# Optimization experiments

Measured on AMD Instinct MI355X. Metric: run time of the kernel, lower is better.

The kernel has to match this reference:

```python
import math
import jax, jax.numpy as jnp
import numpy as np

B, T, C, H = 2, 4096, 512, 8  # batch, seq_len, n_embd, n_head
D = C // H                    # head_dim = 64

def setup_inputs() -> dict:
    key = jax.random.key(0)
    k1, k2, k3 = jax.random.split(key, 3)
    x = jax.random.normal(k1, (B, T, C), dtype=jnp.float32)
    # torch Linear(C, 3C, bias=False): y = x @ W.T; we store the transposed
    # weight directly so the forward is x @ W_attn.
    W_attn = jax.random.normal(k2, (C, 3 * C), dtype=jnp.float32) * 0.02
    W_proj = jax.random.normal(k3, (C, C), dtype=jnp.float32) * 0.02
    return {"x": x, "W_attn": W_attn, "W_proj": W_proj}

def reference(x, W_attn, W_proj):
    b, t, c = x.shape
    # fused QKV projection, split like .split(n_embd, dim=2)
    qkv = x @ W_attn                              # [B,T,3C]
    q, k, v = jnp.split(qkv, 3, axis=-1)          # each [B,T,C]
    def to_heads(u):
        return u.reshape(b, t, H, D).transpose(0, 2, 1, 3)  # [B,H,T,D]
    q, k, v = to_heads(q), to_heads(k), to_heads(v)
    scale = 1.0 / math.sqrt(D)
    att = jnp.einsum('bhqd,bhkd->bhqk', q, k) * scale       # [B,H,T,T]
    causal = jnp.tril(jnp.ones((t, t), dtype=bool))         # masked_fill(triu(...,1), -inf)
    att = jnp.where(causal, att, -jnp.inf)
    probs = jax.nn.softmax(att, axis=-1)
    y = jnp.einsum('bhqk,bhkd->bhqd', probs, v)             # [B,H,T,D]
    y = y.transpose(0, 2, 1, 3).reshape(b, t, c)            # [B,T,C]
    return y @ W_proj
```

## Files before the change

### kernel.cpp

```cpp
#include <hip/hip_runtime.h>
#include <hip/hip_bf16.h>
#include <stdint.h>


typedef __attribute__((ext_vector_type(8))) short short8;
typedef __attribute__((ext_vector_type(4))) float floatx4;
typedef __attribute__((ext_vector_type(16))) float floatx16;
#if __has_builtin(__builtin_amdgcn_permlane32_swap)
typedef __attribute__((ext_vector_type(2))) unsigned int uint2v;
#define HAVE_PLSWAP 1
#else
#define HAVE_PLSWAP 0
#endif

__device__ __forceinline__ unsigned short f2bf(float f) {
    unsigned int x = __float_as_uint(f);
    unsigned int r = x + 0x7fffu + ((x >> 16) & 1u);
    return (unsigned short)(r >> 16);
}

__device__ __forceinline__ unsigned int pk_bf16(float a, float b) {
    __hip_bfloat162 p = __float22bfloat162_rn(make_float2(a, b));
    return *reinterpret_cast<unsigned int*>(&p);
}

__device__ __forceinline__ void gl_lds16(const unsigned short* g, unsigned char* l) {
    __builtin_amdgcn_global_load_lds(
        (const __attribute__((address_space(1))) unsigned int*)g,
        (__attribute__((address_space(3))) unsigned int*)l, 16, 0, 0);
}

__global__ __launch_bounds__(256) void prep_a(
    const float* __restrict__ x, unsigned short* __restrict__ xb,
    const float* __restrict__ Wa, unsigned short* __restrict__ WaT)
{
    const int bid = blockIdx.x;
    const int tid = threadIdx.x;
    if (bid < 2048) {
        size_t i = ((size_t)bid * 256 + tid) * 8;
        float4 a = *reinterpret_cast<const float4*>(x + i);
        float4 b = *reinterpret_cast<const float4*>(x + i + 4);
        unsigned short o[8] = {f2bf(a.x), f2bf(a.y), f2bf(a.z), f2bf(a.w),
                               f2bf(b.x), f2bf(b.y), f2bf(b.z), f2bf(b.w)};
        *reinterpret_cast<uint4*>(xb + i) = *reinterpret_cast<uint4*>(o);
    } else {
        __shared__ unsigned short tile[32][34];
        const int t2 = bid - 2048;
        const int n0 = (t2 % 48) * 32, k0 = (t2 / 48) * 32;
        const int tx = tid & 31, ty = tid >> 5;
        #pragma unroll
        for (int p = 0; p < 4; ++p)
            tile[tx][ty + p * 8] = f2bf(Wa[(size_t)(k0 + ty + p * 8) * 1536 + n0 + tx]);
        __syncthreads();
        #pragma unroll
        for (int p = 0; p < 4; ++p)
            WaT[(size_t)(n0 + ty + p * 8) * 512 + k0 + tx] = tile[ty + p * 8][tx];
    }
}

__global__ __launch_bounds__(256) void transpose_wp(
    const float* __restrict__ W, unsigned short* __restrict__ Wt)
{
    __shared__ unsigned short tile[32][34];
    const int tid = threadIdx.x;
    const int tx = tid & 31, ty = tid >> 5;
    const int n0 = blockIdx.x * 32, k0 = blockIdx.y * 32;
    #pragma unroll
    for (int p = 0; p < 4; ++p)
        tile[tx][ty + p * 8] = f2bf(W[(size_t)(k0 + ty + p * 8) * 512 + n0 + tx]);
    __syncthreads();
    #pragma unroll
    for (int p = 0; p < 4; ++p)
        Wt[(size_t)(n0 + ty + p * 8) * 512 + k0 + tx] = tile[ty + p * 8][tx];
}

template<int EPI>
__global__ __launch_bounds__(256) void mm_bt(
    const unsigned short* __restrict__ A,
    const unsigned short* __restrict__ Bt,
    void* __restrict__ outp)
{
    __shared__ __align__(16) unsigned char smem[40960];

    const int tid  = threadIdx.x;
    const int wave = tid >> 6;
    const int lane = tid & 63;
    const int quad = lane >> 4;
    const int l16  = lane & 15;
    const int wr   = wave >> 1;
    const int wc   = wave & 1;
    const int m0 = blockIdx.x * 128;
    const int n0 = blockIdx.y * 128;

    floatx4 acc[4][4];
    #pragma unroll
    for (int i = 0; i < 4; ++i)
        #pragma unroll
        for (int j = 0; j < 4; ++j) acc[i][j] = (floatx4){0.f, 0.f, 0.f, 0.f};

    const unsigned short* aS = A  + (size_t)(m0 + wave * 16 + (lane >> 2)) * 512 + (lane & 3) * 8;
    const unsigned short* bS = Bt + (size_t)(n0 + wave * 16 + (lane >> 2)) * 512 + (lane & 3) * 8;

#define STAGE(K0S, BUF)                                                     \
    {   unsigned char* Ab = smem + (BUF) * 16384 + wave * 1024;             \
        gl_lds16(aS + (K0S),             Ab);                               \
        gl_lds16(aS + (K0S) + 64 * 512,  Ab + 4096);                        \
        gl_lds16(bS + (K0S),             Ab + 8192);                        \
        gl_lds16(bS + (K0S) + 64 * 512,  Ab + 12288);                       \
    }

    STAGE(0, 0);

    for (int it = 0; it < 16; ++it) {
        __syncthreads();
        if (it < 15) STAGE((it + 1) * 32, (it & 1) ^ 1);

        const unsigned char* Al = smem + (it & 1) * 16384;
        const unsigned char* Bl = Al + 8192;

        short8 af[4], bf[4];
        #pragma unroll
        for (int ti = 0; ti < 4; ++ti)
            af[ti] = *reinterpret_cast<const short8*>(
                Al + (wr * 64 + ti * 16 + l16) * 64 + quad * 16);
        #pragma unroll
        for (int tj = 0; tj < 4; ++tj)
            bf[tj] = *reinterpret_cast<const short8*>(
                Bl + (wc * 64 + tj * 16 + l16) * 64 + quad * 16);
        #pragma unroll
        for (int ti = 0; ti < 4; ++ti)
            #pragma unroll
            for (int tj = 0; tj < 4; ++tj)
                acc[ti][tj] = __builtin_amdgcn_mfma_f32_16x16x32_bf16(af[ti], bf[tj], acc[ti][tj], 0, 0, 0);
    }
#undef STAGE

    if (EPI == 0) {
        unsigned short* WS = (unsigned short*)outp;
        unsigned short* Qb  = WS;
        unsigned short* Kb  = WS + 4194304;
        unsigned short* Vtb = WS + 8388608;
        const int which = n0 >> 9;
        const int h = ((n0 + wc * 64) >> 6) & 7;

        if (which == 2) {
            auto Tr = reinterpret_cast<unsigned short(*)[80]>(smem);
            __syncthreads();
            #pragma unroll
            for (int ti = 0; ti < 4; ++ti)
                #pragma unroll
                for (int tj = 0; tj < 4; ++tj) {
                    unsigned int lo = pk_bf16(acc[ti][tj][0], acc[ti][tj][1]);
                    unsigned int hi = pk_bf16(acc[ti][tj][2], acc[ti][tj][3]);
                    *reinterpret_cast<uint2*>(&Tr[(wave << 6) + tj * 16 + l16][ti * 16 + quad * 4])
                        = make_uint2(lo, hi);
                }
            const int b = m0 >> 12;
            const int bh = b * 8 + h;
            const int t0g = (m0 & 4095) + wr * 64;
            const int tseg = (lane & 7) * 8;
            #pragma unroll
            for (int p = 0; p < 8; ++p) {
                int dl = p * 8 + (lane >> 3);
                uint4 v = *reinterpret_cast<const uint4*>(&Tr[(wave << 6) + dl][tseg]);
                *reinterpret_cast<uint4*>(&Vtb[((size_t)(bh * 64 + dl)) * 4096 + t0g + tseg]) = v;
            }
        } else {
            const float sc = (which == 0) ? 0.18033688f : 1.0f;
            #pragma unroll
            for (int ti = 0; ti < 4; ++ti) {
                #pragma unroll
                for (int r = 0; r < 4; ++r) {
                    int m = m0 + wr * 64 + ti * 16 + quad * 4 + r;
                    int b = m >> 12, t = m & 4095;
                    int bh = b * 8 + h;
                    #pragma unroll
                    for (int tj = 0; tj < 4; ++tj) {
                        int d = tj * 16 + l16;
                        unsigned short val = f2bf(acc[ti][tj][r] * sc);
                        if (which == 0) Qb[((size_t)bh * 4096 + t) * 64 + d] = val;
                        else            Kb[((size_t)bh * 4096 + t) * 64 + d] = val;
                    }
                }
            }
        }
    } else {
        float* Out = (float*)outp;
        #pragma unroll
        for (int ti = 0; ti < 4; ++ti) {
            #pragma unroll
            for (int r = 0; r < 4; ++r) {
                int m = m0 + wr * 64 + ti * 16 + quad * 4 + r;
                #pragma unroll
                for (int tj = 0; tj < 4; ++tj) {
                    int n = n0 + wc * 64 + tj * 16 + l16;
                    Out[(size_t)m * 512 + n] = acc[ti][tj][r];
                }
            }
        }
    }
}

__global__ __launch_bounds__(256) void attn_mfma(
    const unsigned short* __restrict__ Q,
    const unsigned short* __restrict__ K,
    const unsigned short* __restrict__ Vt,
    unsigned short* __restrict__ Y)
{
    __shared__ __align__(16) unsigned short Kc[2][64][64];
    __shared__ __align__(16) unsigned short Vc[2][64][64];

    const int tid  = threadIdx.x;
    const int wave = tid >> 6;
    const int lane = tid & 63;
    const int l32  = lane & 31;
    const int hh   = lane >> 5;
    const int swz  = l32 & 7;
    const int p    = wave >> 1;
    const int w    = wave & 1;

    const int bid = blockIdx.x;
    const int bh  = bid & 15;
    const int j   = (bid >> 4) & 15;
    const int g   = bid >> 8;
    const int qb  = (g == 0) ? j : (g == 1) ? (63 - j) : (g == 2) ? (16 + j) : (47 - j);
    const int m0  = qb * 64;

    const unsigned short* Qp = Q  + (size_t)bh * (4096 * 64);
    const unsigned short* Kp = K  + (size_t)bh * (4096 * 64);
    const unsigned short* Vp = Vt + (size_t)bh * (64 * 4096);

    short8 qf[4];
    #pragma unroll
    for (int k16 = 0; k16 < 4; ++k16)
        qf[k16] = *reinterpret_cast<const short8*>(
            &Qp[(size_t)(m0 + 32 * p + l32) * 64 + k16 * 16 + hh * 8]);

    short8 ones;
    #pragma unroll
    for (int i = 0; i < 8; ++i) ones[i] = (short)0x3F80;

    floatx16 o0 = {0,0,0,0,0,0,0,0,0,0,0,0,0,0,0,0};
    floatx16 o1 = {0,0,0,0,0,0,0,0,0,0,0,0,0,0,0,0};
    floatx16 o4 = {0,0,0,0,0,0,0,0,0,0,0,0,0,0,0,0};

    const int rr  = tid >> 3;
    const int cc  = tid & 7;
    const int c0  = cc * 8;
    const int scs = ((cc ^ (rr & 7)) << 3);

    uint4 rk0 = *reinterpret_cast<const uint4*>(&Kp[(size_t)rr * 64 + c0]);
    uint4 rk1 = *reinterpret_cast<const uint4*>(&Kp[(size_t)(rr + 32) * 64 + c0]);
    uint4 rv0 = *reinterpret_cast<const uint4*>(&Vp[(size_t)rr * 4096 + c0]);
    uint4 rv1 = *reinterpret_cast<const uint4*>(&Vp[(size_t)(rr + 32) * 4096 + c0]);
    *reinterpret_cast<uint4*>(&Kc[0][rr][scs])      = rk0;
    *reinterpret_cast<uint4*>(&Kc[0][rr + 32][scs]) = rk1;
    *reinterpret_cast<uint4*>(&Vc[0][rr][scs])      = rv0;
    *reinterpret_cast<uint4*>(&Vc[0][rr + 32][scs]) = rv1;

    const unsigned short* kq0 = Kp + (size_t)(64 + rr) * 64 + c0;
    const unsigned short* kq1 = Kp + (size_t)(64 + rr + 32) * 64 + c0;
    const unsigned short* vq0 = Vp + (size_t)rr * 4096 + 64 + c0;
    const unsigned short* vq1 = Vp + (size_t)(rr + 32) * 4096 + 64 + c0;

    const int NT = qb + 1;
    for (int kt = 0; kt < NT; ++kt) {
        __syncthreads();
        const int cur = kt & 1;
        const int nxt = cur ^ 1;

        if (kt + 1 < NT) {
            rk0 = *reinterpret_cast<const uint4*>(kq0);
            rk1 = *reinterpret_cast<const uint4*>(kq1);
            rv0 = *reinterpret_cast<const uint4*>(vq0);
            rv1 = *reinterpret_cast<const uint4*>(vq1);
            kq0 += 4096; kq1 += 4096; vq0 += 64; vq1 += 64;
        }

        const bool active = (kt < qb) || (w == 0) || (p == 1);
        if (active) {
            floatx16 s = {0,0,0,0,0,0,0,0,0,0,0,0,0,0,0,0};
            #pragma unroll
            for (int k16 = 0; k16 < 4; ++k16) {
                const int chs = ((2 * k16 + hh) ^ swz) << 3;
                short8 a = *reinterpret_cast<const short8*>(&Kc[cur][32 * w + l32][chs]);
                s = __builtin_amdgcn_mfma_f32_32x32x16_bf16(a, qf[k16], s, 0, 0, 0);
            }
            if (kt == qb) {
                const int ql = 32 * p + l32;
                #pragma unroll
                for (int r = 0; r < 16; ++r) {
                    const int kl = 32 * w + (r & 3) + 8 * (r >> 2) + 4 * hh;
                    s[r] = (kl <= ql) ? s[r] : -1e30f;
                }
            }
            #pragma unroll
            for (int r = 0; r < 16; ++r) s[r] = __builtin_amdgcn_exp2f(s[r]);

            unsigned int A0 = pk_bf16(s[0],  s[1]),  B0 = pk_bf16(s[2],  s[3]);
            unsigned int A1 = pk_bf16(s[4],  s[5]),  B1 = pk_bf16(s[6],  s[7]);
            unsigned int A2 = pk_bf16(s[8],  s[9]),  B2 = pk_bf16(s[10], s[11]);
            unsigned int A3 = pk_bf16(s[12], s[13]), B3 = pk_bf16(s[14], s[15]);
            short8 pa[2];
#if HAVE_PLSWAP
            {
                uint2v rA = __builtin_amdgcn_permlane32_swap(A0, A1, false, false);
                uint2v rB = __builtin_amdgcn_permlane32_swap(B0, B1, false, false);
                uint4 u0 = make_uint4(rA[0], rB[0], rA[1], rB[1]);
                pa[0] = *reinterpret_cast<short8*>(&u0);
                rA = __builtin_amdgcn_permlane32_swap(A2, A3, false, false);
                rB = __builtin_amdgcn_permlane32_swap(B2, B3, false, false);
                uint4 u1 = make_uint4(rA[0], rB[0], rA[1], rB[1]);
                pa[1] = *reinterpret_cast<short8*>(&u1);
            }
#else
            {
                unsigned int pA0 = __shfl_xor((int)A0, 32), pA1 = __shfl_xor((int)A1, 32);
                unsigned int pB0 = __shfl_xor((int)B0, 32), pB1 = __shfl_xor((int)B1, 32);
                unsigned int pA2 = __shfl_xor((int)A2, 32), pA3 = __shfl_xor((int)A3, 32);
                unsigned int pB2 = __shfl_xor((int)B2, 32), pB3 = __shfl_xor((int)B3, 32);
                uint4 u0 = make_uint4(hh ? pA1 : A0, hh ? pB1 : B0,
                                      hh ? A1 : pA0, hh ? B1 : pB0);
                pa[0] = *reinterpret_cast<short8*>(&u0);
                uint4 u1 = make_uint4(hh ? pA3 : A2, hh ? pB3 : B2,
                                      hh ? A3 : pA2, hh ? B3 : pB2);
                pa[1] = *reinterpret_cast<short8*>(&u1);
            }
#endif
            o4 = __builtin_amdgcn_mfma_f32_32x32x16_bf16(pa[0], ones, o4, 0, 0, 0);
            o4 = __builtin_amdgcn_mfma_f32_32x32x16_bf16(pa[1], ones, o4, 0, 0, 0);

            #pragma unroll
            for (int f = 0; f < 2; ++f) {
                const int chs = ((4 * w + 2 * f + hh) ^ swz) << 3;
                short8 b0 = *reinterpret_cast<const short8*>(&Vc[cur][l32][chs]);
                short8 b1 = *reinterpret_cast<const short8*>(&Vc[cur][32 + l32][chs]);
                o0 = __builtin_amdgcn_mfma_f32_32x32x16_bf16(pa[f], b0, o0, 0, 0, 0);
                o1 = __builtin_amdgcn_mfma_f32_32x32x16_bf16(pa[f], b1, o1, 0, 0, 0);
            }
        }

        if (kt + 1 < NT) {
            *reinterpret_cast<uint4*>(&Kc[nxt][rr][scs])      = rk0;
            *reinterpret_cast<uint4*>(&Kc[nxt][rr + 32][scs]) = rk1;
            *reinterpret_cast<uint4*>(&Vc[nxt][rr][scs])      = rv0;
            *reinterpret_cast<uint4*>(&Vc[nxt][rr + 32][scs]) = rv1;
        }
    }

    __syncthreads();
    float* Ob  = reinterpret_cast<float*>(&Kc[0][0][0]);
    float* Wsf = reinterpret_cast<float*>(&Vc[0][0][0]);
    if (l32 == 0) {
        #pragma unroll
        for (int r = 0; r < 16; ++r) {
            const int qloc = (r & 3) + 8 * (r >> 2) + 4 * hh;
            Wsf[(p * 2 + w) * 32 + qloc] = o4[r];
        }
    }
    #pragma unroll
    for (int r = 0; r < 16; ++r) {
        const int qloc = (r & 3) + 8 * (r >> 2) + 4 * hh;
        Ob[((p * 2 + w) * 32 + qloc) * 32 + l32] = w ? o0[r] : o1[r];
    }
    __syncthreads();

    const int b = bh >> 3, h = bh & 7;
    #pragma unroll
    for (int gg = 0; gg < 4; ++gg) {
        float4 a4 = *reinterpret_cast<const float4*>(&Wsf[(p * 2 + 0) * 32 + 8 * gg + 4 * hh]);
        float4 b4 = *reinterpret_cast<const float4*>(&Wsf[(p * 2 + 1) * 32 + 8 * gg + 4 * hh]);
        const float ra[4] = {a4.x + b4.x, a4.y + b4.y, a4.z + b4.z, a4.w + b4.w};
        #pragma unroll
        for (int rsub = 0; rsub < 4; ++rsub) {
            const int r = gg * 4 + rsub;
            const int qloc = 8 * gg + 4 * hh + rsub;
            const float cmb = (w ? o1[r] : o0[r])
                            + Ob[((p * 2 + (1 - w)) * 32 + qloc) * 32 + l32];
            const int t = m0 + 32 * p + qloc;
            Y[((size_t)(b * 4096 + t)) * 512 + h * 64 + 32 * w + l32]
                = f2bf(cmb / ra[rsub]);
        }
    }
}

extern "C" void kernel_launch(void* const* d_in, const int* in_sizes, int n_in,
                              void* d_out, int out_size, void* d_ws, size_t ws_size,
                              hipStream_t stream) {
    const float* x  = (const float*)d_in[0];
    const float* Wa = (const float*)d_in[1];
    const float* Wp = (const float*)d_in[2];
    float* out = (float*)d_out;
    unsigned short* ws = (unsigned short*)d_ws;

    unsigned short* Qb  = ws;
    unsigned short* Kb  = ws + 4194304;
    unsigned short* Vtb = ws + 8388608;
    unsigned short* Yb  = ws + 12582912;
    unsigned short* WaT = Yb;
    unsigned short* WpT = Qb;
    unsigned short* xb  = (unsigned short*)d_out;

    prep_a<<<dim3(2816), dim3(256), 0, stream>>>(x, xb, Wa, WaT);
    mm_bt<0><<<dim3(64, 12), dim3(256), 0, stream>>>(xb, WaT, (void*)ws);
    attn_mfma<<<dim3(1024), dim3(256), 0, stream>>>(Qb, Kb, Vtb, Yb);
    transpose_wp<<<dim3(16, 16), dim3(256), 0, stream>>>(Wp, WpT);
    mm_bt<1><<<dim3(64, 4), dim3(256), 0, stream>>>(Yb, WpT, (void*)out);
}
```

Measured before the change: 163.7 us.

## Pair low and high causal query blocks per workgroup with split-KV merge

Each 512-thread workgroup now handles a light query block and its mirrored heavy block (pp and 63-pp). Both wave groups first process the light block together. They then split the heavy block's remaining key tiles between them and merge the partial sums through shared memory. This balances causal work per block and halves the grid. In exchange it adds more complex staging, extra barriers and a cross-group reduction, and it uses more LDS per block.

```diff
diff --git a/kernel.cpp b/kernel.cpp
--- a/kernel.cpp
+++ b/kernel.cpp
@@ -28,6 +28,73 @@
     __builtin_amdgcn_global_load_lds(
         (const __attribute__((address_space(1))) unsigned int*)g,
         (__attribute__((address_space(3))) unsigned int*)l, 16, 0, 0);
+}
+
+__device__ __forceinline__ void attn_tile(
+    const unsigned short* __restrict__ Kbuf,
+    const unsigned short* __restrict__ Vbuf,
+    const short8* qf, const short8& ones, bool dg,
+    int l32, int hh, int swz, int w, int p2,
+    floatx16& o0, floatx16& o1, floatx16& o4)
+{
+    floatx16 s = {0,0,0,0,0,0,0,0,0,0,0,0,0,0,0,0};
+    #pragma unroll
+    for (int k16 = 0; k16 < 4; ++k16) {
+        const int chs = ((2 * k16 + hh) ^ swz) << 3;
+        short8 a = *reinterpret_cast<const short8*>(&Kbuf[(32 * w + l32) * 64 + chs]);
+        s = __builtin_amdgcn_mfma_f32_32x32x16_bf16(a, qf[k16], s, 0, 0, 0);
+    }
+    if (dg) {
+        const int ql = 32 * p2 + l32;
+        #pragma unroll
+        for (int r = 0; r < 16; ++r) {
+            const int kl = 32 * w + (r & 3) + 8 * (r >> 2) + 4 * hh;
+            s[r] = (kl <= ql) ? s[r] : -1e30f;
+        }
+    }
+    #pragma unroll
+    for (int r = 0; r < 16; ++r) s[r] = __builtin_amdgcn_exp2f(s[r]);
+
+    unsigned int A0 = pk_bf16(s[0],  s[1]),  B0 = pk_bf16(s[2],  s[3]);
+    unsigned int A1 = pk_bf16(s[4],  s[5]),  B1 = pk_bf16(s[6],  s[7]);
+    unsigned int A2 = pk_bf16(s[8],  s[9]),  B2 = pk_bf16(s[10], s[11]);
+    unsigned int A3 = pk_bf16(s[12], s[13]), B3 = pk_bf16(s[14], s[15]);
+    short8 pa[2];
+#if HAVE_PLSWAP
+    {
+        uint2v rA = __builtin_amdgcn_permlane32_swap(A0, A1, false, false);
+        uint2v rB = __builtin_amdgcn_permlane32_swap(B0, B1, false, false);
+        uint4 u0 = make_uint4(rA[0], rB[0], rA[1], rB[1]);
+        pa[0] = *reinterpret_cast<short8*>(&u0);
+        rA = __builtin_amdgcn_permlane32_swap(A2, A3, false, false);
+        rB = __builtin_amdgcn_permlane32_swap(B2, B3, false, false);
+        uint4 u1 = make_uint4(rA[0], rB[0], rA[1], rB[1]);
+        pa[1] = *reinterpret_cast<short8*>(&u1);
+    }
+#else
+    {
+        unsigned int pA0 = __shfl_xor((int)A0, 32), pA1 = __shfl_xor((int)A1, 32);
+        unsigned int pB0 = __shfl_xor((int)B0, 32), pB1 = __shfl_xor((int)B1, 32);
+        unsigned int pA2 = __shfl_xor((int)A2, 32), pA3 = __shfl_xor((int)A3, 32);
+        unsigned int pB2 = __shfl_xor((int)B2, 32), pB3 = __shfl_xor((int)B3, 32);
+        uint4 u0 = make_uint4(hh ? pA1 : A0, hh ? pB1 : B0,
+                              hh ? A1 : pA0, hh ? B1 : pB0);
+        pa[0] = *reinterpret_cast<short8*>(&u0);
+        uint4 u1 = make_uint4(hh ? pA3 : A2, hh ? pB3 : B2,
+                              hh ? A3 : pA2, hh ? B3 : pB2);
+        pa[1] = *reinterpret_cast<short8*>(&u1);
+    }
+#endif
+    o4 = __builtin_amdgcn_mfma_f32_32x32x16_bf16(pa[0], ones, o4, 0, 0, 0);
+    o4 = __builtin_amdgcn_mfma_f32_32x32x16_bf16(pa[1], ones, o4, 0, 0, 0);
+    #pragma unroll
+    for (int f = 0; f < 2; ++f) {
+        const int chs = ((4 * w + 2 * f + hh) ^ swz) << 3;
+        short8 b0 = *reinterpret_cast<const short8*>(&Vbuf[l32 * 64 + chs]);
+        short8 b1 = *reinterpret_cast<const short8*>(&Vbuf[(32 + l32) * 64 + chs]);
+        o0 = __builtin_amdgcn_mfma_f32_32x32x16_bf16(pa[f], b0, o0, 0, 0, 0);
+        o1 = __builtin_amdgcn_mfma_f32_32x32x16_bf16(pa[f], b1, o1, 0, 0, 0);
+    }
 }
 
 __global__ __launch_bounds__(256) void prep_a(
@@ -201,14 +268,13 @@
     }
 }
 
-__global__ __launch_bounds__(256) void attn_mfma(
+__global__ __launch_bounds__(512, 4) void attn_mfma(
     const unsigned short* __restrict__ Q,
     const unsigned short* __restrict__ K,
     const unsigned short* __restrict__ Vt,
     unsigned short* __restrict__ Y)
 {
-    __shared__ __align__(16) unsigned short Kc[2][64][64];
-    __shared__ __align__(16) unsigned short Vc[2][64][64];
+    __shared__ __align__(16) unsigned short smem[4][2][64][64];
 
     const int tid  = threadIdx.x;
     const int wave = tid >> 6;
@@ -216,29 +282,30 @@
     const int l32  = lane & 31;
     const int hh   = lane >> 5;
     const int swz  = l32 & 7;
-    const int p    = wave >> 1;
+    const int qg   = wave >> 2;
+    const int p2   = (wave >> 1) & 1;
     const int w    = wave & 1;
 
     const int bid = blockIdx.x;
     const int bh  = bid & 15;
-    const int j   = (bid >> 4) & 15;
-    const int g   = bid >> 8;
-    const int qb  = (g == 0) ? j : (g == 1) ? (63 - j) : (g == 2) ? (16 + j) : (47 - j);
-    const int m0  = qb * 64;
+    const int pp  = bid >> 4;
+    const int qbL = pp, qbH = 63 - pp;
 
     const unsigned short* Qp = Q  + (size_t)bh * (4096 * 64);
     const unsigned short* Kp = K  + (size_t)bh * (4096 * 64);
     const unsigned short* Vp = Vt + (size_t)bh * (64 * 4096);
-
+    const int b = bh >> 3, h = bh & 7;
+
+    short8 ones;
+    #pragma unroll
+    for (int i = 0; i < 8; ++i) ones[i] = (short)0x3F80;
+
+    const int myqb1 = qg ? qbH : qbL;
     short8 qf[4];
     #pragma unroll
     for (int k16 = 0; k16 < 4; ++k16)
         qf[k16] = *reinterpret_cast<const short8*>(
-            &Qp[(size_t)(m0 + 32 * p + l32) * 64 + k16 * 16 + hh * 8]);
-
-    short8 ones;
-    #pragma unroll
-    for (int i = 0; i < 8; ++i) ones[i] = (short)0x3F80;
+            &Qp[(size_t)(myqb1 * 64 + 32 * p2 + l32) * 64 + k16 * 16 + hh * 8]);
 
     floatx16 o0 = {0,0,0,0,0,0,0,0,0,0,0,0,0,0,0,0};
     floatx16 o1 = {0,0,0,0,0,0,0,0,0,0,0,0,0,0,0,0};
@@ -249,137 +316,195 @@
     const int c0  = cc * 8;
     const int scs = ((cc ^ (rr & 7)) << 3);
 
-    uint4 rk0 = *reinterpret_cast<const uint4*>(&Kp[(size_t)rr * 64 + c0]);
-    uint4 rk1 = *reinterpret_cast<const uint4*>(&Kp[(size_t)(rr + 32) * 64 + c0]);
-    uint4 rv0 = *reinterpret_cast<const uint4*>(&Vp[(size_t)rr * 4096 + c0]);
-    uint4 rv1 = *reinterpret_cast<const uint4*>(&Vp[(size_t)(rr + 32) * 4096 + c0]);
-    *reinterpret_cast<uint4*>(&Kc[0][rr][scs])      = rk0;
-    *reinterpret_cast<uint4*>(&Kc[0][rr + 32][scs]) = rk1;
-    *reinterpret_cast<uint4*>(&Vc[0][rr][scs])      = rv0;
-    *reinterpret_cast<uint4*>(&Vc[0][rr + 32][scs]) = rv1;
-
-    const unsigned short* kq0 = Kp + (size_t)(64 + rr) * 64 + c0;
-    const unsigned short* kq1 = Kp + (size_t)(64 + rr + 32) * 64 + c0;
-    const unsigned short* vq0 = Vp + (size_t)rr * 4096 + 64 + c0;
-    const unsigned short* vq1 = Vp + (size_t)(rr + 32) * 4096 + 64 + c0;
-
-    const int NT = qb + 1;
-    for (int kt = 0; kt < NT; ++kt) {
+    {
+        uint4 k0v = *reinterpret_cast<const uint4*>(&Kp[(size_t)rr * 64 + c0]);
+        uint4 v0v = *reinterpret_cast<const uint4*>(&Vp[(size_t)rr * 4096 + c0]);
+        *reinterpret_cast<uint4*>(&smem[0][0][rr][scs]) = k0v;
+        *reinterpret_cast<uint4*>(&smem[0][1][rr][scs]) = v0v;
+    }
+
+    uint4 rk, rv;
+    for (int s = 0; s <= pp; ++s) {
         __syncthreads();
-        const int cur = kt & 1;
-        const int nxt = cur ^ 1;
-
-        if (kt + 1 < NT) {
-            rk0 = *reinterpret_cast<const uint4*>(kq0);
-            rk1 = *reinterpret_cast<const uint4*>(kq1);
-            rv0 = *reinterpret_cast<const uint4*>(vq0);
-            rv1 = *reinterpret_cast<const uint4*>(vq1);
-            kq0 += 4096; kq1 += 4096; vq0 += 64; vq1 += 64;
-        }
-
-        const bool active = (kt < qb) || (w == 0) || (p == 1);
-        if (active) {
-            floatx16 s = {0,0,0,0,0,0,0,0,0,0,0,0,0,0,0,0};
-            #pragma unroll
-            for (int k16 = 0; k16 < 4; ++k16) {
-                const int chs = ((2 * k16 + hh) ^ swz) << 3;
-                short8 a = *reinterpret_cast<const short8*>(&Kc[cur][32 * w + l32][chs]);
-                s = __builtin_amdgcn_mfma_f32_32x32x16_bf16(a, qf[k16], s, 0, 0, 0);
-            }
-            if (kt == qb) {
-                const int ql = 32 * p + l32;
+        const int cur = s & 1;
+        if (s < pp) {
+            rk = *reinterpret_cast<const uint4*>(&Kp[(size_t)((s + 1) * 64 + rr) * 64 + c0]);
+            rv = *reinterpret_cast<const uint4*>(&Vp[(size_t)rr * 4096 + (s + 1) * 64 + c0]);
+        }
+        attn_tile(&smem[cur][0][0][0], &smem[cur][1][0][0], qf, ones,
+                  (qg == 0) && (s == pp), l32, hh, swz, w, p2, o0, o1, o4);
+        if (s < pp) {
+            *reinterpret_cast<uint4*>(&smem[cur ^ 1][0][rr][scs]) = rk;
+            *reinterpret_cast<uint4*>(&smem[cur ^ 1][1][rr][scs]) = rv;
+        }
+    }
+
+    __syncthreads();
+    {
+        float* ObM  = reinterpret_cast<float*>(&smem[0][0][0][0]);
+        float* WsfM = reinterpret_cast<float*>(&smem[1][0][0][0]);
+        const int local = tid & 255;
+        if (qg == 0) {
+            const int lw = p2 * 2 + w;
+            if (l32 == 0) {
                 #pragma unroll
                 for (int r = 0; r < 16; ++r) {
-                    const int kl = 32 * w + (r & 3) + 8 * (r >> 2) + 4 * hh;
-                    s[r] = (kl <= ql) ? s[r] : -1e30f;
+                    const int qloc = (r & 3) + 8 * (r >> 2) + 4 * hh;
+                    WsfM[lw * 32 + qloc] = o4[r];
                 }
             }
             #pragma unroll
-            for (int r = 0; r < 16; ++r) s[r] = __builtin_amdgcn_exp2f(s[r]);
-
-            unsigned int A0 = pk_bf16(s[0],  s[1]),  B0 = pk_bf16(s[2],  s[3]);
-            unsigned int A1 = pk_bf16(s[4],  s[5]),  B1 = pk_bf16(s[6],  s[7]);
-            unsigned int A2 = pk_bf16(s[8],  s[9]),  B2 = pk_bf16(s[10], s[11]);
-            unsigned int A3 = pk_bf16(s[12], s[13]), B3 = pk_bf16(s[14], s[15]);
-            short8 pa[2];
-#if HAVE_PLSWAP
-            {
-                uint2v rA = __builtin_amdgcn_permlane32_swap(A0, A1, false, false);
-                uint2v rB = __builtin_amdgcn_permlane32_swap(B0, B1, false, false);
-                uint4 u0 = make_uint4(rA[0], rB[0], rA[1], rB[1]);
-                pa[0] = *reinterpret_cast<short8*>(&u0);
-                rA = __builtin_amdgcn_permlane32_swap(A2, A3, false, false);
-                rB = __builtin_amdgcn_permlane32_swap(B2, B3, false, false);
-                uint4 u1 = make_uint4(rA[0], rB[0], rA[1], rB[1]);
-                pa[1] = *reinterpret_cast<short8*>(&u1);
-            }
-#else
-            {
-                unsigned int pA0 = __shfl_xor((int)A0, 32), pA1 = __shfl_xor((int)A1, 32);
-                unsigned int pB0 = __shfl_xor((int)B0, 32), pB1 = __shfl_xor((int)B1, 32);
-                unsigned int pA2 = __shfl_xor((int)A2, 32), pA3 = __shfl_xor((int)A3, 32);
-                unsigned int pB2 = __shfl_xor((int)B2, 32), pB3 = __shfl_xor((int)B3, 32);
-                uint4 u0 = make_uint4(hh ? pA1 : A0, hh ? pB1 : B0,
-                                      hh ? A1 : pA0, hh ? B1 : pB0);
-                pa[0] = *reinterpret_cast<short8*>(&u0);
-                uint4 u1 = make_uint4(hh ? pA3 : A2, hh ? pB3 : B2,
-                                      hh ? A3 : pA2, hh ? B3 : pB2);
-                pa[1] = *reinterpret_cast<short8*>(&u1);
-            }
-#endif
-            o4 = __builtin_amdgcn_mfma_f32_32x32x16_bf16(pa[0], ones, o4, 0, 0, 0);
-            o4 = __builtin_amdgcn_mfma_f32_32x32x16_bf16(pa[1], ones, o4, 0, 0, 0);
-
-            #pragma unroll
-            for (int f = 0; f < 2; ++f) {
-                const int chs = ((4 * w + 2 * f + hh) ^ swz) << 3;
-                short8 b0 = *reinterpret_cast<const short8*>(&Vc[cur][l32][chs]);
-                short8 b1 = *reinterpret_cast<const short8*>(&Vc[cur][32 + l32][chs]);
-                o0 = __builtin_amdgcn_mfma_f32_32x32x16_bf16(pa[f], b0, o0, 0, 0, 0);
-                o1 = __builtin_amdgcn_mfma_f32_32x32x16_bf16(pa[f], b1, o1, 0, 0, 0);
-            }
-        }
-
-        if (kt + 1 < NT) {
-            *reinterpret_cast<uint4*>(&Kc[nxt][rr][scs])      = rk0;
-            *reinterpret_cast<uint4*>(&Kc[nxt][rr + 32][scs]) = rk1;
-            *reinterpret_cast<uint4*>(&Vc[nxt][rr][scs])      = rv0;
-            *reinterpret_cast<uint4*>(&Vc[nxt][rr + 32][scs]) = rv1;
+            for (int r = 0; r < 16; ++r) {
+                const int qloc = (r & 3) + 8 * (r >> 2) + 4 * hh;
+                ObM[(lw * 32 + qloc) * 32 + l32] = w ? o0[r] : o1[r];
+            }
+        } else {
+            const int rr2 = local >> 3, cc2 = local & 7;
+            const int c02 = cc2 * 8;
+            const int sc2 = ((cc2 ^ (rr2 & 7)) << 3);
+            const int tA = pp + 1;
+            const int tB = (pp + 2 > 63) ? 63 : pp + 2;
+            uint4 x0 = *reinterpret_cast<const uint4*>(&Kp[(size_t)(tA * 64 + rr2) * 64 + c02]);
+            uint4 x1 = *reinterpret_cast<const uint4*>(&Kp[(size_t)(tA * 64 + rr2 + 32) * 64 + c02]);
+            uint4 x2 = *reinterpret_cast<const uint4*>(&Vp[(size_t)rr2 * 4096 + tA * 64 + c02]);
+            uint4 x3 = *reinterpret_cast<const uint4*>(&Vp[(size_t)(rr2 + 32) * 4096 + tA * 64 + c02]);
+            *reinterpret_cast<uint4*>(&smem[2][0][rr2][sc2])      = x0;
+            *reinterpret_cast<uint4*>(&smem[2][0][rr2 + 32][sc2]) = x1;
+            *reinterpret_cast<uint4*>(&smem[2][1][rr2][sc2])      = x2;
+            *reinterpret_cast<uint4*>(&smem[2][1][rr2 + 32][sc2]) = x3;
+            x0 = *reinterpret_cast<const uint4*>(&Kp[(size_t)(tB * 64 + rr2) * 64 + c02]);
+            x1 = *reinterpret_cast<const uint4*>(&Kp[(size_t)(tB * 64 + rr2 + 32) * 64 + c02]);
+            x2 = *reinterpret_cast<const uint4*>(&Vp[(size_t)rr2 * 4096 + tB * 64 + c02]);
+            x3 = *reinterpret_cast<const uint4*>(&Vp[(size_t)(rr2 + 32) * 4096 + tB * 64 + c02]);
+            *reinterpret_cast<uint4*>(&smem[3][0][rr2][sc2])      = x0;
+            *reinterpret_cast<uint4*>(&smem[3][0][rr2 + 32][sc2]) = x1;
+            *reinterpret_cast<uint4*>(&smem[3][1][rr2][sc2])      = x2;
+            *reinterpret_cast<uint4*>(&smem[3][1][rr2 + 32][sc2]) = x3;
+        }
+        __syncthreads();
+        if (qg == 0) {
+            const int m0L = qbL * 64;
+            #pragma unroll
+            for (int gg = 0; gg < 4; ++gg) {
+                float4 a4 = *reinterpret_cast<const float4*>(&WsfM[(p2 * 2 + 0) * 32 + 8 * gg + 4 * hh]);
+                float4 b4 = *reinterpret_cast<const float4*>(&WsfM[(p2 * 2 + 1) * 32 + 8 * gg + 4 * hh]);
+                const float ra[4] = {a4.x + b4.x, a4.y + b4.y, a4.z + b4.z, a4.w + b4.w};
+                #pragma unroll
+                for (int rsub = 0; rsub < 4; ++rsub) {
+                    const int r = gg * 4 + rsub;
+                    const int qloc = 8 * gg + 4 * hh + rsub;
+                    const float cmb = (w ? o1[r] : o0[r])
+                                    + ObM[((p2 * 2 + (1 - w)) * 32 + qloc) * 32 + l32];
+                    const int t = m0L + 32 * p2 + qloc;
+                    Y[((size_t)(b * 4096 + t)) * 512 + h * 64 + 32 * w + l32]
+                        = f2bf(cmb / ra[rsub]);
+                }
+            }
+            #pragma unroll
+            for (int k16 = 0; k16 < 4; ++k16)
+                qf[k16] = *reinterpret_cast<const short8*>(
+                    &Qp[(size_t)(qbH * 64 + 32 * p2 + l32) * 64 + k16 * 16 + hh * 8]);
+            #pragma unroll
+            for (int r = 0; r < 16; ++r) { o0[r] = 0.f; o1[r] = 0.f; o4[r] = 0.f; }
+        }
+    }
+
+    const int S2  = 32 - pp;
+    const int rr2 = (tid & 255) >> 3;
+    const int cc2 = (tid & 255) & 7;
+    const int c02 = cc2 * 8;
+    const int sc2 = ((cc2 ^ (rr2 & 7)) << 3);
+    const int tsel = tid >> 8;
+    uint4 f0, f1, f2, f3;
+    for (int s = 1; s <= S2; ++s) {
+        __syncthreads();
+        const int base = (s & 1) ? 2 : 0;
+        if (s < S2) {
+            int tn = pp + 2 * s + 1 + tsel;
+            if (tn > 63) tn = 63;
+            f0 = *reinterpret_cast<const uint4*>(&Kp[(size_t)(tn * 64 + rr2) * 64 + c02]);
+            f1 = *reinterpret_cast<const uint4*>(&Kp[(size_t)(tn * 64 + rr2 + 32) * 64 + c02]);
+            f2 = *reinterpret_cast<const uint4*>(&Vp[(size_t)rr2 * 4096 + tn * 64 + c02]);
+            f3 = *reinterpret_cast<const uint4*>(&Vp[(size_t)(rr2 + 32) * 4096 + tn * 64 + c02]);
+        }
+        if (qg == 1) {
+            attn_tile(&smem[base][0][0][0], &smem[base][1][0][0], qf, ones,
+                      s == S2, l32, hh, swz, w, p2, o0, o1, o4);
+        } else if (s < S2) {
+            attn_tile(&smem[base + 1][0][0][0], &smem[base + 1][1][0][0], qf, ones,
+                      false, l32, hh, swz, w, p2, o0, o1, o4);
+        }
+        if (s < S2) {
+            const int tb = (base ^ 2) + tsel;
+            *reinterpret_cast<uint4*>(&smem[tb][0][rr2][sc2])      = f0;
+            *reinterpret_cast<uint4*>(&smem[tb][0][rr2 + 32][sc2]) = f1;
+            *reinterpret_cast<uint4*>(&smem[tb][1][rr2][sc2])      = f2;
+            *reinterpret_cast<uint4*>(&smem[tb][1][rr2 + 32][sc2]) = f3;
         }
     }
 
     __syncthreads();
-    float* Ob  = reinterpret_cast<float*>(&Kc[0][0][0]);
-    float* Wsf = reinterpret_cast<float*>(&Vc[0][0][0]);
-    if (l32 == 0) {
+    float* Lo  = reinterpret_cast<float*>(&smem[0][0][0][0]);
+    float* Lrs = reinterpret_cast<float*>(&smem[2][0][0][0]);
+    if (qg == 0) {
+        const int lw = p2 * 2 + w;
         #pragma unroll
         for (int r = 0; r < 16; ++r) {
             const int qloc = (r & 3) + 8 * (r >> 2) + 4 * hh;
-            Wsf[(p * 2 + w) * 32 + qloc] = o4[r];
-        }
-    }
-    #pragma unroll
-    for (int r = 0; r < 16; ++r) {
-        const int qloc = (r & 3) + 8 * (r >> 2) + 4 * hh;
-        Ob[((p * 2 + w) * 32 + qloc) * 32 + l32] = w ? o0[r] : o1[r];
+            Lo[(lw * 32 + qloc) * 64 + l32]      = o0[r];
+            Lo[(lw * 32 + qloc) * 64 + 32 + l32] = o1[r];
+        }
+        if (l32 == 0) {
+            #pragma unroll
+            for (int r = 0; r < 16; ++r) {
+                const int qloc = (r & 3) + 8 * (r >> 2) + 4 * hh;
+                Lrs[lw * 32 + qloc] = o4[r];
+            }
+        }
     }
     __syncthreads();
-
-    const int b = bh >> 3, h = bh & 7;
-    #pragma unroll
-    for (int gg = 0; gg < 4; ++gg) {
-        float4 a4 = *reinterpret_cast<const float4*>(&Wsf[(p * 2 + 0) * 32 + 8 * gg + 4 * hh]);
-        float4 b4 = *reinterpret_cast<const float4*>(&Wsf[(p * 2 + 1) * 32 + 8 * gg + 4 * hh]);
-        const float ra[4] = {a4.x + b4.x, a4.y + b4.y, a4.z + b4.z, a4.w + b4.w};
-        #pragma unroll
-        for (int rsub = 0; rsub < 4; ++rsub) {
-            const int r = gg * 4 + rsub;
-            const int qloc = 8 * gg + 4 * hh + rsub;
-            const float cmb = (w ? o1[r] : o0[r])
-                            + Ob[((p * 2 + (1 - w)) * 32 + qloc) * 32 + l32];
-            const int t = m0 + 32 * p + qloc;
-            Y[((size_t)(b * 4096 + t)) * 512 + h * 64 + 32 * w + l32]
-                = f2bf(cmb / ra[rsub]);
+    float* Ob2 = reinterpret_cast<float*>(&smem[3][0][0][0]);
+    float* Ws2 = reinterpret_cast<float*>(&smem[2][1][0][0]);
+    if (qg == 1) {
+        const int lw = p2 * 2 + w;
+        #pragma unroll
+        for (int r = 0; r < 16; ++r) {
+            const int qloc = (r & 3) + 8 * (r >> 2) + 4 * hh;
+            o0[r] += Lo[(lw * 32 + qloc) * 64 + l32];
+            o1[r] += Lo[(lw * 32 + qloc) * 64 + 32 + l32];
+            o4[r] += Lrs[lw * 32 + qloc];
+        }
+        if (l32 == 0) {
+            #pragma unroll
+            for (int r = 0; r < 16; ++r) {
+                const int qloc = (r & 3) + 8 * (r >> 2) + 4 * hh;
+                Ws2[lw * 32 + qloc] = o4[r];
+            }
+        }
+        #pragma unroll
+        for (int r = 0; r < 16; ++r) {
+            const int qloc = (r & 3) + 8 * (r >> 2) + 4 * hh;
+            Ob2[(lw * 32 + qloc) * 32 + l32] = w ? o0[r] : o1[r];
+        }
+    }
+    __syncthreads();
+    if (qg == 1) {
+        const int m0H = qbH * 64;
+        #pragma unroll
+        for (int gg = 0; gg < 4; ++gg) {
+            float4 a4 = *reinterpret_cast<const float4*>(&Ws2[(p2 * 2 + 0) * 32 + 8 * gg + 4 * hh]);
+            float4 b4 = *reinterpret_cast<const float4*>(&Ws2[(p2 * 2 + 1) * 32 + 8 * gg + 4 * hh]);
+            const float ra[4] = {a4.x + b4.x, a4.y + b4.y, a4.z + b4.z, a4.w + b4.w};
+            #pragma unroll
+            for (int rsub = 0; rsub < 4; ++rsub) {
+                const int r = gg * 4 + rsub;
+                const int qloc = 8 * gg + 4 * hh + rsub;
+                const float cmb = (w ? o1[r] : o0[r])
+                                + Ob2[((p2 * 2 + (1 - w)) * 32 + qloc) * 32 + l32];
+                const int t = m0H + 32 * p2 + qloc;
+                Y[((size_t)(b * 4096 + t)) * 512 + h * 64 + 32 * w + l32]
+                    = f2bf(cmb / ra[rsub]);
+            }
         }
     }
 }
@@ -403,7 +528,7 @@
 
     prep_a<<<dim3(2816), dim3(256), 0, stream>>>(x, xb, Wa, WaT);
     mm_bt<0><<<dim3(64, 12), dim3(256), 0, stream>>>(xb, WaT, (void*)ws);
-    attn_mfma<<<dim3(1024), dim3(256), 0, stream>>>(Qb, Kb, Vtb, Yb);
+    attn_mfma<<<dim3(512), dim3(512), 0, stream>>>(Qb, Kb, Vtb, Yb);
     transpose_wp<<<dim3(16, 16), dim3(256), 0, stream>>>(Wp, WpT);
     mm_bt<1><<<dim3(64, 4), dim3(256), 0, stream>>>(Yb, WpT, (void*)out);
 }
```

Result: faster. 157.8 us (-3.6%).
